# Kernel tuning notes

Hardware: AMD Instinct MI355X
Metric: run time of the kernel (lower is better)

The kernel has to match this reference:

```python
import jax, jax.numpy as jnp
import numpy as np

B, S, D = 8, 2048, 1024
NEG_INF = jnp.float32(-1e30)  # stand-in for -inf; rows with all-masked are overwritten anyway


def setup_inputs() -> dict:
    key = jax.random.key(0)
    ks = jax.random.split(key, 10)
    query = jax.random.normal(ks[0], (B, S, D), dtype=jnp.float32)
    key_t = jax.random.normal(ks[1], (B, S, D), dtype=jnp.float32)
    value = jax.random.normal(ks[2], (B, S, D), dtype=jnp.float32)
    # pad mask: prefix of valid tokens per batch element (realistic ragged batch)
    lengths = jax.random.randint(ks[3], (B,), S // 2, S + 1)
    pad_masks = jnp.arange(S)[None, :] < lengths[:, None]  # (B, S) bool
    # causal mask, same lower-triangular pattern per batch element
    causal = jnp.tril(jnp.ones((S, S), dtype=bool))
    causal_masks = jnp.broadcast_to(causal, (B, S, S))
    # Linear params (torch nn.Linear: y = x @ W.T + b)
    scale = 0.02
    Wq = jax.random.normal(ks[4], (D, D), dtype=jnp.float32) * scale
    bq = jnp.zeros((D,), dtype=jnp.float32)
    Wk = jax.random.normal(ks[5], (D, D), dtype=jnp.float32) * scale
    bk = jnp.zeros((D,), dtype=jnp.float32)
    Wv = jax.random.normal(ks[6], (D, D), dtype=jnp.float32) * scale
    bv = jnp.zeros((D,), dtype=jnp.float32)
    return {"query": query, "key": key_t, "value": value,
            "pad_masks": pad_masks, "causal_masks": causal_masks,
            "Wq": Wq, "bq": bq, "Wk": Wk, "bk": bk, "Wv": Wv, "bv": bv}


def reference(query, key, value, pad_masks, causal_masks, Wq, bq, Wk, bk, Wv, bv):
    d_model = query.shape[-1]
    Q = jnp.einsum('bsd,ed->bse', query, Wq) + bq
    K = jnp.einsum('bsd,ed->bse', key, Wk) + bk
    V = jnp.einsum('bsd,ed->bse', value, Wv) + bv
    scores = jnp.einsum('bqd,bkd->bqk', Q, K) / jnp.sqrt(jnp.float32(d_model))
    combined = pad_masks[:, None, :] & causal_masks              # (B, S, S)
    row_any = jnp.any(combined, axis=-1, keepdims=True)          # (B, S, 1)
    scores = jnp.where(combined, scores, NEG_INF)
    scores = jnp.where(row_any, scores, jnp.zeros_like(scores))
    attn = jax.nn.softmax(scores, axis=-1)
    attn = jnp.where(row_any, attn, jnp.zeros_like(attn))
    # multiply by pad mask along the QUERY axis (faithful to the torch transpose)
    attn = attn * pad_masks[:, :, None].astype(attn.dtype)
    seq_emds = jnp.einsum('bqk,bkd->bqd', attn, V)
    return seq_emds, attn
```

## Files before the change

kernel.cpp:

```cpp
#include <hip/hip_runtime.h>
#include <hip/hip_bf16.h>

#define B_ 8
#define S_ 2048
#define D_ 1024
#define SCALE 0.03125f
#define NT_ (D_ / 64)

typedef __attribute__((ext_vector_type(4))) float f32x4;
typedef __attribute__((ext_vector_type(8))) short short8;
typedef __attribute__((ext_vector_type(4))) short short4v;

static __device__ inline unsigned short f2bf(float f) {
    unsigned int u = __float_as_uint(f);
    u += 0x7FFF + ((u >> 16) & 1);
    return (unsigned short)(u >> 16);
}

static __device__ __forceinline__ void gload16(const void* g, void* l) {
    __builtin_amdgcn_global_load_lds(
        (const __attribute__((address_space(1))) unsigned int*)g,
        (__attribute__((address_space(3))) unsigned int*)l, 16, 0, 0);
}

static __device__ __forceinline__ void pipe_sync() {
    asm volatile("s_waitcnt vmcnt(0)" ::: "memory");
    __builtin_amdgcn_s_barrier();
    __builtin_amdgcn_sched_barrier(0);
}

static __device__ __forceinline__ int xcd_swz(int hw, int nwg) {
    return (hw & 7) * (nwg >> 3) + (hw >> 3);
}

static __device__ __forceinline__ int swz(int byte) {
    return byte ^ (((byte >> 7) & 7) << 4);
}

__global__ void lengths_kernel(const unsigned char* __restrict__ pm, int* __restrict__ lens) {
    __shared__ int cnt[B_];
    int tid = threadIdx.x;
    if (tid < B_) cnt[tid] = 0;
    __syncthreads();
    int layout;
    if (pm[0] == 1 && pm[1] == 1) layout = 0;
    else if (pm[0] == 1) layout = 1;
    else layout = 2;
    for (int i = tid; i < B_ * S_; i += blockDim.x) {
        bool v;
        if (layout == 0) v = pm[i] != 0;
        else if (layout == 1) v = ((const int*)pm)[i] != 0;
        else v = ((const float*)pm)[i] != 0.0f;
        if (v) atomicAdd(&cnt[i >> 11], 1);
    }
    __syncthreads();
    if (tid < B_) lens[tid] = cnt[tid];
}

__global__ void convert_all_kernel(const float* __restrict__ q, const float* __restrict__ k,
                                   const float* __restrict__ v,
                                   const float* __restrict__ Wq, const float* __restrict__ Wk,
                                   const float* __restrict__ Wv,
                                   unsigned short* __restrict__ Xb,
                                   unsigned short* __restrict__ Wb) {
    const int z = blockIdx.z;
    const float* src;
    unsigned short* dst;
    int n;
    if (z < 3) {
        src = (z == 0) ? q : (z == 1) ? k : v;
        dst = Xb + (size_t)z * B_ * S_ * D_;
        n = B_ * S_ * D_;
    } else {
        src = (z == 3) ? Wq : (z == 4) ? Wk : Wv;
        dst = Wb + (size_t)(z - 3) * D_ * D_;
        n = D_ * D_;
    }
    int idx = (blockIdx.x * 256 + threadIdx.x) * 8;
    if (idx >= n) return;
    float4 a = *(const float4*)(src + idx);
    float4 b = *(const float4*)(src + idx + 4);
    short8 o;
    o[0] = (short)f2bf(a.x); o[1] = (short)f2bf(a.y);
    o[2] = (short)f2bf(a.z); o[3] = (short)f2bf(a.w);
    o[4] = (short)f2bf(b.x); o[5] = (short)f2bf(b.y);
    o[6] = (short)f2bf(b.z); o[7] = (short)f2bf(b.w);
    *(short8*)(dst + idx) = o;
}

__global__ __launch_bounds__(512, 1) void proj2_kernel(
        const unsigned short* __restrict__ Xb3,
        const unsigned short* __restrict__ Wb3,
        const float* __restrict__ bq, const float* __restrict__ bk,
        const float* __restrict__ bv,
        unsigned short* __restrict__ Qb,
        unsigned short* __restrict__ Kb,
        unsigned short* __restrict__ Vt) {
    const int nwg = 3 * (B_ * S_ / 256) * (D_ / 256);
    const int log_id = xcd_swz(blockIdx.x, nwg);
    const int z = log_id >> 8;
    const int rem = log_id & 255;
    const int m0 = (rem >> 2) * 256;
    const int n0 = (rem & 3) * 256;

    const unsigned short* Xb = Xb3 + (size_t)z * B_ * S_ * D_;
    const unsigned short* Wb = Wb3 + (size_t)z * D_ * D_;
    const float* bias = (z == 0) ? bq : (z == 1) ? bk : bv;

    __shared__ unsigned short lds[2][2][2][128 * 64];

    const int tid = threadIdx.x;
    const int lane = tid & 63, wid = tid >> 6;
    const int wm = wid >> 2, wn = wid & 3;
    const int g = lane >> 4, l15 = lane & 15;

    const int f0 = tid * 16;
    const int r0s = f0 >> 7, c0s = f0 & 127;
    const int csrc = c0s ^ ((r0s & 7) << 4);

    f32x4 acc[8][4];
    const f32x4 z4 = {0.f, 0.f, 0.f, 0.f};
#pragma unroll
    for (int a = 0; a < 8; ++a)
#pragma unroll
        for (int b2 = 0; b2 < 4; ++b2) acc[a][b2] = z4;

    auto stageT = [&](int buf, int kk) {
#pragma unroll
        for (int h = 0; h < 2; ++h) {
            gload16((const char*)Xb + ((size_t)(m0 + h * 128 + r0s) * D_ + kk) * 2 + csrc,
                    (char*)&lds[buf][0][h][0] + f0);
            gload16((const char*)Xb + ((size_t)(m0 + h * 128 + r0s + 64) * D_ + kk) * 2 + csrc,
                    (char*)&lds[buf][0][h][0] + f0 + 8192);
            gload16((const char*)Wb + ((size_t)(n0 + h * 128 + r0s) * D_ + kk) * 2 + csrc,
                    (char*)&lds[buf][1][h][0] + f0);
            gload16((const char*)Wb + ((size_t)(n0 + h * 128 + r0s + 64) * D_ + kk) * 2 + csrc,
                    (char*)&lds[buf][1][h][0] + f0 + 8192);
        }
    };

    stageT(0, 0);
    pipe_sync();

    for (int T = 0; T < NT_; ++T) {
        const int buf = T & 1;
        if (T + 1 < NT_) stageT(buf ^ 1, (T + 1) * 64);
        const char* Abase = (const char*)&lds[buf][0][wm][0];
#pragma unroll
        for (int ks = 0; ks < 2; ++ks) {
            const int colb = ks * 64 + g * 16;
            short8 bfr[4], afr[8];
#pragma unroll
            for (int nf = 0; nf < 4; ++nf) {
                int nl = wn * 64 + nf * 16 + l15;
                bfr[nf] = *(const short8*)((const char*)&lds[buf][1][nl >> 7][0]
                                           + swz((nl & 127) * 128 + colb));
            }
#pragma unroll
            for (int mf = 0; mf < 8; ++mf)
                afr[mf] = *(const short8*)(Abase + swz((mf * 16 + l15) * 128 + colb));
            __builtin_amdgcn_s_setprio(1);
#pragma unroll
            for (int mf = 0; mf < 8; ++mf)
#pragma unroll
                for (int nf = 0; nf < 4; ++nf)
                    acc[mf][nf] = __builtin_amdgcn_mfma_f32_16x16x32_bf16(
                        afr[mf], bfr[nf], acc[mf][nf], 0, 0, 0);
            __builtin_amdgcn_s_setprio(0);
        }
        pipe_sync();
    }

    if (z < 2) {
        unsigned short* O = (z == 0) ? Qb : Kb;
#pragma unroll
        for (int mf = 0; mf < 8; ++mf) {
#pragma unroll
            for (int nf = 0; nf < 4; ++nf) {
                int gm = m0 + wm * 128 + mf * 16 + 4 * g;
                int gn = n0 + wn * 64 + nf * 16 + l15;
                float bb = bias[gn];
#pragma unroll
                for (int i = 0; i < 4; ++i)
                    O[(size_t)(gm + i) * D_ + gn] = f2bf(acc[mf][nf][i] + bb);
            }
        }
    } else {
#pragma unroll
        for (int mf = 0; mf < 8; ++mf) {
#pragma unroll
            for (int nf = 0; nf < 4; ++nf) {
                int gm = m0 + wm * 128 + mf * 16 + 4 * g;
                int b = gm >> 11, tok = gm & 2047;
                int gn = n0 + wn * 64 + nf * 16 + l15;
                float bb = bias[gn];
                short4v sv;
#pragma unroll
                for (int i = 0; i < 4; ++i) sv[i] = (short)f2bf(acc[mf][nf][i] + bb);
                *(short4v*)(&Vt[((size_t)b * D_ + gn) * S_ + tok]) = sv;
            }
        }
    }
}

__global__ void proj_kernel(const float* __restrict__ q, const float* __restrict__ k,
                            const float* __restrict__ v,
                            const float* __restrict__ Wq, const float* __restrict__ Wk,
                            const float* __restrict__ Wv,
                            const float* __restrict__ bq, const float* __restrict__ bk,
                            const float* __restrict__ bv,
                            unsigned short* __restrict__ Qb, unsigned short* __restrict__ Kb,
                            unsigned short* __restrict__ Vt) {
    const int z = blockIdx.z;
    const float* X = (z == 0) ? q : (z == 1) ? k : v;
    const float* W = (z == 0) ? Wq : (z == 1) ? Wk : Wv;
    const float* bias = (z == 0) ? bq : (z == 1) ? bk : bv;

    __shared__ short As[128 * 40];
    __shared__ short Bs[128 * 40];

    const int m0 = blockIdx.y * 128;
    const int n0 = blockIdx.x * 128;
    const int tid = threadIdx.x;
    const int lane = tid & 63, wid = tid >> 6;
    const int wr = wid >> 1, wc = wid & 1;
    const int g = lane >> 4, l15 = lane & 15;

    f32x4 acc[4][4];
    const f32x4 z4 = {0.f, 0.f, 0.f, 0.f};
    for (int a = 0; a < 4; ++a)
        for (int b2 = 0; b2 < 4; ++b2) acc[a][b2] = z4;

    for (int kk = 0; kk < D_; kk += 32) {
#pragma unroll
        for (int it = 0; it < 4; ++it) {
            int flat = it * 1024 + tid * 4;
            int r = flat >> 5, c = flat & 31;
            float4 va = *(const float4*)(X + (size_t)(m0 + r) * D_ + kk + c);
            short4v sa = {(short)f2bf(va.x), (short)f2bf(va.y), (short)f2bf(va.z), (short)f2bf(va.w)};
            *(short4v*)(&As[r * 40 + c]) = sa;
            float4 vb = *(const float4*)(W + (size_t)(n0 + r) * D_ + kk + c);
            short4v sb = {(short)f2bf(vb.x), (short)f2bf(vb.y), (short)f2bf(vb.z), (short)f2bf(vb.w)};
            *(short4v*)(&Bs[r * 40 + c]) = sb;
        }
        __syncthreads();
        short8 a_frag[4], b_frag[4];
#pragma unroll
        for (int mf = 0; mf < 4; ++mf)
            a_frag[mf] = *(const short8*)(&As[(wr * 64 + mf * 16 + l15) * 40 + g * 8]);
#pragma unroll
        for (int nf = 0; nf < 4; ++nf)
            b_frag[nf] = *(const short8*)(&Bs[(wc * 64 + nf * 16 + l15) * 40 + g * 8]);
#pragma unroll
        for (int mf = 0; mf < 4; ++mf)
#pragma unroll
            for (int nf = 0; nf < 4; ++nf)
                acc[mf][nf] = __builtin_amdgcn_mfma_f32_16x16x32_bf16(a_frag[mf], b_frag[nf], acc[mf][nf], 0, 0, 0);
        __syncthreads();
    }

    if (z < 2) {
        unsigned short* O = (z == 0) ? Qb : Kb;
#pragma unroll
        for (int mf = 0; mf < 4; ++mf) {
#pragma unroll
            for (int nf = 0; nf < 4; ++nf) {
                int gm = m0 + wr * 64 + mf * 16 + 4 * g;
                int gn = n0 + wc * 64 + nf * 16 + l15;
                float bb = bias[gn];
#pragma unroll
                for (int i = 0; i < 4; ++i)
                    O[(size_t)(gm + i) * D_ + gn] = f2bf(acc[mf][nf][i] + bb);
            }
        }
    } else {
#pragma unroll
        for (int mf = 0; mf < 4; ++mf) {
#pragma unroll
            for (int nf = 0; nf < 4; ++nf) {
                int gm = m0 + wr * 64 + mf * 16 + 4 * g;
                int b = gm >> 11, tok = gm & 2047;
                int gn = n0 + wc * 64 + nf * 16 + l15;
                float bb = bias[gn];
                short4v sv;
#pragma unroll
                for (int i = 0; i < 4; ++i) sv[i] = (short)f2bf(acc[mf][nf][i] + bb);
                *(short4v*)(&Vt[((size_t)b * D_ + gn) * S_ + tok]) = sv;
            }
        }
    }
}

__global__ void scores_kernel(const unsigned short* __restrict__ Qb,
                              const unsigned short* __restrict__ Kb,
                              const int* __restrict__ lens,
                              float* __restrict__ attn) {
    const int log_id = xcd_swz(blockIdx.x, 136 * B_);
    const int b = log_id / 136;
    const int idx = log_id - b * 136;
    int qt = (int)((sqrtf(8.f * idx + 1.f) - 1.f) * 0.5f);
    while ((qt + 1) * (qt + 2) / 2 <= idx) ++qt;
    while (qt * (qt + 1) / 2 > idx) --qt;
    const int kt = idx - qt * (qt + 1) / 2;
    const int m0 = qt * 128, n0 = kt * 128;
    const int len = lens[b];
    if (m0 >= len) return;

    __shared__ unsigned short As[2][128 * 64];
    __shared__ unsigned short Bs[2][128 * 64];

    const int tid = threadIdx.x;
    const int lane = tid & 63, w = tid >> 6;
    const int wr = w >> 1, wc = w & 1;
    const int g = lane >> 4, l15 = lane & 15;

    const char* Qbase = (const char*)(Qb + (size_t)(b * S_ + m0) * D_);
    const char* Kbase = (const char*)(Kb + (size_t)(b * S_ + n0) * D_);

    const int f0 = tid * 16;
    const int rs = f0 >> 7, cs = f0 & 127;
    const int csrc = cs ^ ((rs & 7) << 4);

    auto stage = [&](int buf, int kk) {
#pragma unroll
        for (int c = 0; c < 4; ++c) {
            gload16(Qbase + (size_t)(rs + c * 32) * (D_ * 2) + kk * 2 + csrc,
                    (char*)&As[buf][0] + c * 4096 + f0);
            gload16(Kbase + (size_t)(rs + c * 32) * (D_ * 2) + kk * 2 + csrc,
                    (char*)&Bs[buf][0] + c * 4096 + f0);
        }
    };

    f32x4 acc[4][4];
    const f32x4 z4 = {0.f, 0.f, 0.f, 0.f};
    for (int a = 0; a < 4; ++a)
        for (int b2 = 0; b2 < 4; ++b2) acc[a][b2] = z4;

    stage(0, 0);
    pipe_sync();
    for (int T = 0; T < NT_; ++T) {
        const int cur = T & 1;
        if (T + 1 < NT_) stage(cur ^ 1, (T + 1) * 64);
#pragma unroll
        for (int ks = 0; ks < 2; ++ks) {
            const int colb = ks * 64 + g * 16;
            short8 a_frag[4], b_frag[4];
#pragma unroll
            for (int mf = 0; mf < 4; ++mf)
                a_frag[mf] = *(const short8*)((const char*)&As[cur][0]
                                              + swz((wr * 64 + mf * 16 + l15) * 128 + colb));
#pragma unroll
            for (int nf = 0; nf < 4; ++nf)
                b_frag[nf] = *(const short8*)((const char*)&Bs[cur][0]
                                              + swz((wc * 64 + nf * 16 + l15) * 128 + colb));
            __builtin_amdgcn_s_setprio(1);
#pragma unroll
            for (int mf = 0; mf < 4; ++mf)
#pragma unroll
                for (int nf = 0; nf < 4; ++nf)
                    acc[mf][nf] = __builtin_amdgcn_mfma_f32_16x16x32_bf16(
                        a_frag[mf], b_frag[nf], acc[mf][nf], 0, 0, 0);
            __builtin_amdgcn_s_setprio(0);
        }
        pipe_sync();
    }

    const bool interior = (m0 >= n0 + 128) && (m0 + 128 <= len);
    if (interior) {
#pragma unroll
        for (int mf = 0; mf < 4; ++mf) {
#pragma unroll
            for (int nf = 0; nf < 4; ++nf) {
                int gm = m0 + wr * 64 + mf * 16 + 4 * g;
                int gn = n0 + wc * 64 + nf * 16 + l15;
#pragma unroll
                for (int i = 0; i < 4; ++i)
                    attn[(size_t)(b * S_ + gm + i) * S_ + gn] = acc[mf][nf][i] * SCALE;
            }
        }
    } else {
#pragma unroll
        for (int mf = 0; mf < 4; ++mf) {
#pragma unroll
            for (int nf = 0; nf < 4; ++nf) {
                int gm = m0 + wr * 64 + mf * 16 + 4 * g;
                int gn = n0 + wc * 64 + nf * 16 + l15;
#pragma unroll
                for (int i = 0; i < 4; ++i) {
                    int rq = gm + i;
                    if (rq < len && gn <= rq)
                        attn[(size_t)(b * S_ + rq) * S_ + gn] = acc[mf][nf][i] * SCALE;
                }
            }
        }
    }
}

__global__ void softmax_kernel(const int* __restrict__ lens,
                               float* __restrict__ attn, unsigned short* __restrict__ P) {
    const int row = blockIdx.x;
    const int b = row >> 11, qpos = row & 2047;
    const int tid = threadIdx.x;
    const size_t rbase = (size_t)row * S_;
    const int c0 = tid * 8;
    const short8 zp = {0, 0, 0, 0, 0, 0, 0, 0};
    const float4 zf = {0.f, 0.f, 0.f, 0.f};
    if (qpos >= lens[b]) {
        *(short8*)(&P[rbase + c0]) = zp;
        *(float4*)(attn + rbase + c0) = zf;
        *(float4*)(attn + rbase + c0 + 4) = zf;
        return;
    }
    __shared__ float wm[4], wl[4];
    const bool act = (c0 <= qpos);
    float x[8];
    if (act) {
        float4 a0 = *(const float4*)(attn + rbase + c0);
        float4 a1 = *(const float4*)(attn + rbase + c0 + 4);
        x[0] = a0.x; x[1] = a0.y; x[2] = a0.z; x[3] = a0.w;
        x[4] = a1.x; x[5] = a1.y; x[6] = a1.z; x[7] = a1.w;
#pragma unroll
        for (int j = 0; j < 8; ++j)
            if (c0 + j > qpos) x[j] = -1e30f;
    } else {
#pragma unroll
        for (int j = 0; j < 8; ++j) x[j] = -1e30f;
    }
    float lmax = -1e30f;
#pragma unroll
    for (int j = 0; j < 8; ++j) lmax = fmaxf(lmax, x[j]);
#pragma unroll
    for (int off = 1; off < 64; off <<= 1) lmax = fmaxf(lmax, __shfl_xor(lmax, off));
    if ((tid & 63) == 0) wm[tid >> 6] = lmax;
    __syncthreads();
    const float m = fmaxf(fmaxf(wm[0], wm[1]), fmaxf(wm[2], wm[3]));
    float e[8];
    float lsum = 0.f;
#pragma unroll
    for (int j = 0; j < 8; ++j) {
        e[j] = (x[j] > -1e29f) ? __expf(x[j] - m) : 0.f;
        lsum += e[j];
    }
#pragma unroll
    for (int off = 1; off < 64; off <<= 1) lsum += __shfl_xor(lsum, off);
    if ((tid & 63) == 0) wl[tid >> 6] = lsum;
    __syncthreads();
    if (act) {
        const float inv = 1.0f / (wl[0] + wl[1] + wl[2] + wl[3]);
        float4 o0, o1;
        short8 pb;
#pragma unroll
        for (int j = 0; j < 8; ++j) {
            e[j] *= inv;
            pb[j] = (short)f2bf(e[j]);
        }
        o0.x = e[0]; o0.y = e[1]; o0.z = e[2]; o0.w = e[3];
        o1.x = e[4]; o1.y = e[5]; o1.z = e[6]; o1.w = e[7];
        *(float4*)(attn + rbase + c0) = o0;
        *(float4*)(attn + rbase + c0 + 4) = o1;
        *(short8*)(&P[rbase + c0]) = pb;
    } else {
        *(float4*)(attn + rbase + c0) = zf;
        *(float4*)(attn + rbase + c0 + 4) = zf;
        *(short8*)(&P[rbase + c0]) = zp;
    }
}

__global__ void pv_kernel(const unsigned short* __restrict__ P,
                          const unsigned short* __restrict__ Vt,
                          const int* __restrict__ lens, float* __restrict__ seq) {
    const int log_id = xcd_swz(blockIdx.x, B_ * (S_ / 128) * (D_ / 128));
    const int b = log_id >> 7;
    const int rem = log_id & 127;
    const int q0 = (rem >> 3) * 128;
    const int n0 = (rem & 7) * 128;
    const int len = lens[b];
    const int tid = threadIdx.x;

    if (q0 >= len) {
        const float4 zf = {0.f, 0.f, 0.f, 0.f};
#pragma unroll
        for (int it = 0; it < 16; ++it) {
            int flat = it * 1024 + tid * 4;
            int r = flat >> 7, c = flat & 127;
            *(float4*)(&seq[(size_t)(b * S_ + q0 + r) * D_ + n0 + c]) = zf;
        }
        return;
    }

    __shared__ unsigned short As[2][128 * 64];
    __shared__ unsigned short Bs[2][128 * 64];
    const int lane = tid & 63, w = tid >> 6;
    const int wr = w >> 1, wc = w & 1;
    const int g = lane >> 4, l15 = lane & 15;

    const char* Pbase = (const char*)(P + (size_t)(b * S_ + q0) * S_);
    const char* Vbase = (const char*)(Vt + ((size_t)b * D_ + n0) * S_);

    const int f0 = tid * 16;
    const int rs = f0 >> 7, cs = f0 & 127;
    const int csrc = cs ^ ((rs & 7) << 4);

    auto stage = [&](int buf, int kk) {
#pragma unroll
        for (int c = 0; c < 4; ++c) {
            gload16(Pbase + (size_t)(rs + c * 32) * (S_ * 2) + kk * 2 + csrc,
                    (char*)&As[buf][0] + c * 4096 + f0);
            gload16(Vbase + (size_t)(rs + c * 32) * (S_ * 2) + kk * 2 + csrc,
                    (char*)&Bs[buf][0] + c * 4096 + f0);
        }
    };

    f32x4 acc[4][4];
    const f32x4 z4 = {0.f, 0.f, 0.f, 0.f};
    for (int a = 0; a < 4; ++a)
        for (int b2 = 0; b2 < 4; ++b2) acc[a][b2] = z4;

    const int nkt = (q0 + 128) / 64;

    stage(0, 0);
    pipe_sync();
    for (int T = 0; T < nkt; ++T) {
        const int cur = T & 1;
        if (T + 1 < nkt) stage(cur ^ 1, (T + 1) * 64);
#pragma unroll
        for (int ks = 0; ks < 2; ++ks) {
            const int colb = ks * 64 + g * 16;
            short8 a_frag[4], b_frag[4];
#pragma unroll
            for (int mf = 0; mf < 4; ++mf)
                a_frag[mf] = *(const short8*)((const char*)&As[cur][0]
                                              + swz((wr * 64 + mf * 16 + l15) * 128 + colb));
#pragma unroll
            for (int nf = 0; nf < 4; ++nf)
                b_frag[nf] = *(const short8*)((const char*)&Bs[cur][0]
                                              + swz((wc * 64 + nf * 16 + l15) * 128 + colb));
            __builtin_amdgcn_s_setprio(1);
#pragma unroll
            for (int mf = 0; mf < 4; ++mf)
#pragma unroll
                for (int nf = 0; nf < 4; ++nf)
                    acc[mf][nf] = __builtin_amdgcn_mfma_f32_16x16x32_bf16(
                        a_frag[mf], b_frag[nf], acc[mf][nf], 0, 0, 0);
            __builtin_amdgcn_s_setprio(0);
        }
        pipe_sync();
    }

#pragma unroll
    for (int mf = 0; mf < 4; ++mf) {
#pragma unroll
        for (int nf = 0; nf < 4; ++nf) {
            int gq = q0 + wr * 64 + mf * 16 + 4 * g;
            int gn = n0 + wc * 64 + nf * 16 + l15;
#pragma unroll
            for (int i = 0; i < 4; ++i)
                seq[(size_t)(b * S_ + gq + i) * D_ + gn] = acc[mf][nf][i];
        }
    }
}

extern "C" void kernel_launch(void* const* d_in, const int* in_sizes, int n_in,
                              void* d_out, int out_size, void* d_ws, size_t ws_size,
                              hipStream_t stream) {
    const float* q = (const float*)d_in[0];
    const float* k = (const float*)d_in[1];
    const float* v = (const float*)d_in[2];
    const unsigned char* pm = (const unsigned char*)d_in[3];
    const float* Wq = (const float*)d_in[5];
    const float* bq = (const float*)d_in[6];
    const float* Wk = (const float*)d_in[7];
    const float* bk = (const float*)d_in[8];
    const float* Wv = (const float*)d_in[9];
    const float* bv = (const float*)d_in[10];

    float* seq = (float*)d_out;
    float* attn = seq + (size_t)B_ * S_ * D_;

    char* ws = (char*)d_ws;
    int* lens = (int*)ws;
    unsigned short* Qb = (unsigned short*)(ws + 256);
    unsigned short* Kb = Qb + (size_t)B_ * S_ * D_;
    unsigned short* Vt = Kb + (size_t)B_ * S_ * D_;
    unsigned short* Xb = Vt + (size_t)B_ * D_ * S_;
    unsigned short* Wb = Xb + 3ull * B_ * S_ * D_;
    unsigned short* P = Qb;

    const size_t need = 256 + 6ull * B_ * S_ * D_ * 2 + 3ull * D_ * D_ * 2;

    lengths_kernel<<<1, 256, 0, stream>>>(pm, lens);

    if (ws_size >= need) {
        convert_all_kernel<<<dim3(B_ * S_ * D_ / 2048, 1, 6), 256, 0, stream>>>(
            q, k, v, Wq, Wk, Wv, Xb, Wb);
        proj2_kernel<<<dim3(3 * (B_ * S_ / 256) * (D_ / 256)), 512, 0, stream>>>(
            Xb, Wb, bq, bk, bv, Qb, Kb, Vt);
    } else {
        proj_kernel<<<dim3(D_ / 128, (B_ * S_) / 128, 3), 256, 0, stream>>>(
            q, k, v, Wq, Wk, Wv, bq, bk, bv, Qb, Kb, Vt);
    }

    scores_kernel<<<dim3(136 * B_), 256, 0, stream>>>(Qb, Kb, lens, attn);
    softmax_kernel<<<dim3(B_ * S_), 256, 0, stream>>>(lens, attn, P);
    pv_kernel<<<dim3(B_ * (S_ / 128) * (D_ / 128)), 256, 0, stream>>>(P, Vt, lens, seq);
}
```

Measured before the change: 386.3 us.

## Fuse fp32-to-bf16 activation conversion into projection GEMM A-tile staging

The separate pass that converted q/k/v activations to bf16 in workspace is removed. The projection GEMM now loads fp32 activation tiles into registers, converts them to bf16, and writes them into swizzled LDS, double-buffered around the MFMA loop, while weights are still converted separately. This removes a full write and re-read of the three bf16 activation copies, at the cost of twice the global read bytes per A tile inside the GEMM and extra VALU conversion and register pressure. pipe_sync now also waits on lgkmcnt so the LDS writes finish before the barrier.

```diff
diff --git a/kernel.cpp b/kernel.cpp
--- a/kernel.cpp
+++ b/kernel.cpp
@@ -24,7 +24,7 @@
 }
 
 static __device__ __forceinline__ void pipe_sync() {
-    asm volatile("s_waitcnt vmcnt(0)" ::: "memory");
+    asm volatile("s_waitcnt vmcnt(0) lgkmcnt(0)" ::: "memory");
     __builtin_amdgcn_s_barrier();
     __builtin_amdgcn_sched_barrier(0);
 }
@@ -57,27 +57,14 @@
     if (tid < B_) lens[tid] = cnt[tid];
 }
 
-__global__ void convert_all_kernel(const float* __restrict__ q, const float* __restrict__ k,
-                                   const float* __restrict__ v,
-                                   const float* __restrict__ Wq, const float* __restrict__ Wk,
-                                   const float* __restrict__ Wv,
-                                   unsigned short* __restrict__ Xb,
-                                   unsigned short* __restrict__ Wb) {
+__global__ void convert_w_kernel(const float* __restrict__ Wq, const float* __restrict__ Wk,
+                                 const float* __restrict__ Wv,
+                                 unsigned short* __restrict__ Wb) {
     const int z = blockIdx.z;
-    const float* src;
-    unsigned short* dst;
-    int n;
-    if (z < 3) {
-        src = (z == 0) ? q : (z == 1) ? k : v;
-        dst = Xb + (size_t)z * B_ * S_ * D_;
-        n = B_ * S_ * D_;
-    } else {
-        src = (z == 3) ? Wq : (z == 4) ? Wk : Wv;
-        dst = Wb + (size_t)(z - 3) * D_ * D_;
-        n = D_ * D_;
-    }
+    const float* src = (z == 0) ? Wq : (z == 1) ? Wk : Wv;
+    unsigned short* dst = Wb + (size_t)z * D_ * D_;
     int idx = (blockIdx.x * 256 + threadIdx.x) * 8;
-    if (idx >= n) return;
+    if (idx >= D_ * D_) return;
     float4 a = *(const float4*)(src + idx);
     float4 b = *(const float4*)(src + idx + 4);
     short8 o;
@@ -88,8 +75,9 @@
     *(short8*)(dst + idx) = o;
 }
 
-__global__ __launch_bounds__(512, 1) void proj2_kernel(
-        const unsigned short* __restrict__ Xb3,
+__global__ __launch_bounds__(512, 1) void proj2f_kernel(
+        const float* __restrict__ q, const float* __restrict__ k,
+        const float* __restrict__ v,
         const unsigned short* __restrict__ Wb3,
         const float* __restrict__ bq, const float* __restrict__ bk,
         const float* __restrict__ bv,
@@ -103,7 +91,7 @@
     const int m0 = (rem >> 2) * 256;
     const int n0 = (rem & 3) * 256;
 
-    const unsigned short* Xb = Xb3 + (size_t)z * B_ * S_ * D_;
+    const float* X = (z == 0) ? q : (z == 1) ? k : v;
     const unsigned short* Wb = Wb3 + (size_t)z * D_ * D_;
     const float* bias = (z == 0) ? bq : (z == 1) ? bk : bv;
 
@@ -118,20 +106,9 @@
     const int r0s = f0 >> 7, c0s = f0 & 127;
     const int csrc = c0s ^ ((r0s & 7) << 4);
 
-    f32x4 acc[8][4];
-    const f32x4 z4 = {0.f, 0.f, 0.f, 0.f};
-#pragma unroll
-    for (int a = 0; a < 8; ++a)
-#pragma unroll
-        for (int b2 = 0; b2 < 4; ++b2) acc[a][b2] = z4;
-
-    auto stageT = [&](int buf, int kk) {
+    auto stageB = [&](int buf, int kk) {
 #pragma unroll
         for (int h = 0; h < 2; ++h) {
-            gload16((const char*)Xb + ((size_t)(m0 + h * 128 + r0s) * D_ + kk) * 2 + csrc,
-                    (char*)&lds[buf][0][h][0] + f0);
-            gload16((const char*)Xb + ((size_t)(m0 + h * 128 + r0s + 64) * D_ + kk) * 2 + csrc,
-                    (char*)&lds[buf][0][h][0] + f0 + 8192);
             gload16((const char*)Wb + ((size_t)(n0 + h * 128 + r0s) * D_ + kk) * 2 + csrc,
                     (char*)&lds[buf][1][h][0] + f0);
             gload16((const char*)Wb + ((size_t)(n0 + h * 128 + r0s + 64) * D_ + kk) * 2 + csrc,
@@ -139,13 +116,50 @@
         }
     };
 
-    stageT(0, 0);
+    const int rA = tid >> 1;
+    const int hA = rA >> 7, rAl = rA & 127;
+    const int c0A = (tid & 1) * 32;
+    const float* Abase_g = X + (size_t)(m0 + rA) * D_ + c0A;
+    f32x4 areg[8];
+
+    auto loadA = [&](int kk) {
+        const float* src = Abase_g + kk;
+#pragma unroll
+        for (int j = 0; j < 8; ++j) areg[j] = *(const f32x4*)(src + j * 4);
+    };
+    auto writeA = [&](int buf) {
+        char* base = (char*)&lds[buf][0][hA][0];
+#pragma unroll
+        for (int j = 0; j < 4; ++j) {
+            short8 o;
+            f32x4 a = areg[2 * j], b = areg[2 * j + 1];
+            o[0] = (short)f2bf(a[0]); o[1] = (short)f2bf(a[1]);
+            o[2] = (short)f2bf(a[2]); o[3] = (short)f2bf(a[3]);
+            o[4] = (short)f2bf(b[0]); o[5] = (short)f2bf(b[1]);
+            o[6] = (short)f2bf(b[2]); o[7] = (short)f2bf(b[3]);
+            *(short8*)(base + swz(rAl * 128 + c0A * 2 + j * 16)) = o;
+        }
+    };
+
+    f32x4 acc[8][4];
+    const f32x4 z4 = {0.f, 0.f, 0.f, 0.f};
+#pragma unroll
+    for (int a = 0; a < 8; ++a)
+#pragma unroll
+        for (int b2 = 0; b2 < 4; ++b2) acc[a][b2] = z4;
+
+    loadA(0);
+    stageB(0, 0);
+    writeA(0);
     pipe_sync();
 
     for (int T = 0; T < NT_; ++T) {
         const int buf = T & 1;
-        if (T + 1 < NT_) stageT(buf ^ 1, (T + 1) * 64);
-        const char* Abase = (const char*)&lds[buf][0][wm][0];
+        if (T + 1 < NT_) {
+            stageB(buf ^ 1, (T + 1) * 64);
+            loadA((T + 1) * 64);
+        }
+        const char* Ab = (const char*)&lds[buf][0][wm][0];
 #pragma unroll
         for (int ks = 0; ks < 2; ++ks) {
             const int colb = ks * 64 + g * 16;
@@ -158,7 +172,7 @@
             }
 #pragma unroll
             for (int mf = 0; mf < 8; ++mf)
-                afr[mf] = *(const short8*)(Abase + swz((mf * 16 + l15) * 128 + colb));
+                afr[mf] = *(const short8*)(Ab + swz((mf * 16 + l15) * 128 + colb));
             __builtin_amdgcn_s_setprio(1);
 #pragma unroll
             for (int mf = 0; mf < 8; ++mf)
@@ -168,6 +182,7 @@
                         afr[mf], bfr[nf], acc[mf][nf], 0, 0, 0);
             __builtin_amdgcn_s_setprio(0);
         }
+        if (T + 1 < NT_) writeA(buf ^ 1);
         pipe_sync();
     }
 
@@ -582,19 +597,17 @@
     unsigned short* Qb = (unsigned short*)(ws + 256);
     unsigned short* Kb = Qb + (size_t)B_ * S_ * D_;
     unsigned short* Vt = Kb + (size_t)B_ * S_ * D_;
-    unsigned short* Xb = Vt + (size_t)B_ * D_ * S_;
-    unsigned short* Wb = Xb + 3ull * B_ * S_ * D_;
+    unsigned short* Wb = Vt + (size_t)B_ * D_ * S_;
     unsigned short* P = Qb;
 
-    const size_t need = 256 + 6ull * B_ * S_ * D_ * 2 + 3ull * D_ * D_ * 2;
+    const size_t need = 256 + 3ull * B_ * S_ * D_ * 2 + 3ull * D_ * D_ * 2;
 
     lengths_kernel<<<1, 256, 0, stream>>>(pm, lens);
 
     if (ws_size >= need) {
-        convert_all_kernel<<<dim3(B_ * S_ * D_ / 2048, 1, 6), 256, 0, stream>>>(
-            q, k, v, Wq, Wk, Wv, Xb, Wb);
-        proj2_kernel<<<dim3(3 * (B_ * S_ / 256) * (D_ / 256)), 512, 0, stream>>>(
-            Xb, Wb, bq, bk, bv, Qb, Kb, Vt);
+        convert_w_kernel<<<dim3(D_ * D_ / 2048, 1, 3), 256, 0, stream>>>(Wq, Wk, Wv, Wb);
+        proj2f_kernel<<<dim3(3 * (B_ * S_ / 256) * (D_ / 256)), 512, 0, stream>>>(
+            q, k, v, Wb, bq, bk, bv, Qb, Kb, Vt);
     } else {
         proj_kernel<<<dim3(D_ / 128, (B_ * S_) / 128, 3), 256, 0, stream>>>(
             q, k, v, Wq, Wk, Wv, bq, bk, bv, Qb, Kb, Vt);
```

Result: slower. 408.1 us (+5.7%).
